# Kernel tuning notes

Measured on AMD Instinct MI355X. Metric: run time of the kernel, lower is better.

The kernel has to match this reference:

```python
import jax, jax.numpy as jnp
import numpy as np

HID = 32          # PositionalEncodingFourier hidden_dim
PE_TEMP = 10000.0


def _layer_norm(x, w, b):
    m = jnp.mean(x, -1, keepdims=True)
    v = jnp.mean((x - m) ** 2, -1, keepdims=True)
    return (x - m) / jnp.sqrt(v + 1e-6) * w + b


def _dwconv(x, w, b):
    # x: (B,C,H,W), w: (C,1,3,3) depthwise
    y = jax.lax.conv_general_dilated(x, w, (1, 1), 'SAME',
                                     feature_group_count=x.shape[1],
                                     dimension_numbers=('NCHW', 'OIHW', 'NCHW'))
    return y + b[None, :, None, None]


def _pos_embed(B, H, W, pw, pb):
    scale = 2 * np.pi
    eps = 1e-6
    dim_t = PE_TEMP ** (2 * (jnp.arange(HID) // 2).astype(jnp.float32) / HID)

    def four(e):  # e: (M,) -> (M,HID), interleaved sin/cos
        p = e[:, None] / dim_t
        return jnp.stack([jnp.sin(p[:, 0::2]), jnp.cos(p[:, 1::2])], -1).reshape(e.shape[0], HID)

    ye = jnp.arange(1, H + 1, dtype=jnp.float32) / (H + eps) * scale
    xe = jnp.arange(1, W + 1, dtype=jnp.float32) / (W + eps) * scale
    py = jnp.broadcast_to(four(ye)[:, None, :], (H, W, HID))
    px = jnp.broadcast_to(four(xe)[None, :, :], (H, W, HID))
    pos = jnp.concatenate([py, px], -1) @ pw.T + pb     # (H,W,C)
    C = pos.shape[-1]
    return jnp.broadcast_to(pos[None], (B, H, W, C)).reshape(B, H * W, C)


def _l2norm(x):
    return x / jnp.maximum(jnp.linalg.norm(x, axis=-1, keepdims=True), 1e-12)


def setup_inputs() -> dict:
    key = jax.random.key(0)
    ks = jax.random.split(key, 10)
    B, C, H, W = 32, 384, 32, 32
    nh, hid = 6, 6 * C
    f32 = jnp.float32
    d = {
        'x': jax.random.normal(ks[0], (B, C, H, W), f32),
        'pos_w': 0.02 * jax.random.normal(ks[1], (C, 2 * HID), f32),
        'pos_b': jnp.zeros((C,), f32),
        'ln1_w': jnp.ones((C,), f32), 'ln1_b': jnp.zeros((C,), f32),
        'q_w': 0.02 * jax.random.normal(ks[2], (C, C), f32), 'q_b': jnp.zeros((C,), f32),
        'k_w': 0.02 * jax.random.normal(ks[3], (C, C), f32), 'k_b': jnp.zeros((C,), f32),
        'vc_w': 0.02 * jax.random.normal(ks[4], (C, C), f32), 'vc_b': jnp.zeros((C,), f32),
        'dw_w': 0.1 * jax.random.normal(ks[5], (C, 1, 3, 3), f32), 'dw_b': jnp.zeros((C,), f32),
        'bn_g': jnp.ones((C,), f32), 'bn_b': jnp.zeros((C,), f32),
        'bn_mean': jnp.zeros((C,), f32), 'bn_var': jnp.ones((C,), f32),
        'temp': jnp.ones((nh, 1, 1), f32),
        'proj_w': 0.02 * jax.random.normal(ks[6], (C, C), f32), 'proj_b': jnp.zeros((C,), f32),
        'gamma1': jnp.full((C,), 1e-6, f32),
        'ln2_w': jnp.ones((C,), f32), 'ln2_b': jnp.zeros((C,), f32),
        'mlp_w1': 0.02 * jax.random.normal(ks[7], (hid, C), f32), 'mlp_b1': jnp.zeros((hid,), f32),
        'mlp_dw': 0.1 * jax.random.normal(ks[8], (hid, 1, 3, 3), f32), 'mlp_db': jnp.zeros((hid,), f32),
        'mlp_w2': 0.02 * jax.random.normal(ks[9], (C, hid), f32), 'mlp_b2': jnp.zeros((C,), f32),
        'gamma2': jnp.full((C,), 1e-6, f32),
    }
    return d


def reference(x, pos_w, pos_b, ln1_w, ln1_b, q_w, q_b, k_w, k_b, vc_w, vc_b,
              dw_w, dw_b, bn_g, bn_b, bn_mean, bn_var, temp, proj_w, proj_b,
              gamma1, ln2_w, ln2_b, mlp_w1, mlp_b1, mlp_dw, mlp_db,
              mlp_w2, mlp_b2, gamma2):
    B, C, H, W = x.shape
    N = H * W
    nh = temp.shape[0]
    dh = C // nh

    xf = x.reshape(B, C, N).transpose(0, 2, 1)          # (B,N,C)
    xf = xf + _pos_embed(B, H, W, pos_w, pos_b)
    xn = _layer_norm(xf, ln1_w, ln1_b)                  # (B,N,C)
    xs = xn.transpose(0, 2, 1).reshape(B, C, H, W)      # spatial view for DWConv

    # --- GLGXCA: channel-wise cross-covariance attention ---
    q = (xn @ q_w.T + q_b).reshape(B, N, nh, dh).transpose(0, 2, 3, 1)  # (B,h,d,N)
    k = (xn @ k_w.T + k_b).reshape(B, N, nh, dh).transpose(0, 2, 3, 1)
    q = _l2norm(q)
    k = _l2norm(k)
    attn = jnp.einsum('bhdn,bhen->bhde', q, k) * temp   # (B,h,d,d)
    attn = jax.nn.softmax(attn, axis=-1)

    vg = _dwconv(xs, dw_w, dw_b)
    vg = (vg - bn_mean[None, :, None, None]) / jnp.sqrt(bn_var + 1e-5)[None, :, None, None] \
         * bn_g[None, :, None, None] + bn_b[None, :, None, None]
    vg = vg * jax.nn.sigmoid(vg)                        # SiLU
    vg = vg.transpose(0, 2, 3, 1).reshape(B, N, C)
    vc = xn @ vc_w.T + vc_b
    v = (vc * vg).reshape(B, N, nh, dh).transpose(0, 2, 3, 1)           # (B,h,d,N)

    xo = jnp.einsum('bhde,bhen->bhdn', attn, v)         # (B,h,d,N)
    xo = xo.transpose(0, 3, 1, 2).reshape(B, N, C)
    xo = xo @ proj_w.T + proj_b
    xo = xo.reshape(B, H, W, C).transpose(0, 3, 1, 2)   # (B,C,H,W)

    # --- residual 1 (faithful: torch does transpose(1,2).reshape on BCHW) ---
    xa = xo * gamma1[None, :, None, None]
    xa = jnp.swapaxes(xa, 1, 2).reshape(B, C, H, W)
    x = x + xa

    # --- MLP branch ---
    xn2 = _layer_norm(x.transpose(0, 2, 3, 1), ln2_w, ln2_b).transpose(0, 3, 1, 2)
    h1 = jnp.einsum('bchw,oc->bohw', xn2, mlp_w1) + mlp_b1[None, :, None, None]
    h1 = jax.nn.gelu(h1, approximate=False)
    h2 = jax.nn.gelu(_dwconv(h1, mlp_dw, mlp_db), approximate=False)
    h3 = jnp.einsum('bchw,oc->bohw', h2, mlp_w2) + mlp_b2[None, :, None, None]
    return x + h3 * gamma2[None, :, None, None]
```

## Files before the change

### kernel.cpp

```cpp
#include <hip/hip_runtime.h>
#include <cstdint>
#include <cstddef>
#include <cmath>

#define DI __device__ __forceinline__

typedef __attribute__((ext_vector_type(2))) float f32x2;
typedef __attribute__((ext_vector_type(4))) float f32x4;
typedef __attribute__((ext_vector_type(8))) __bf16 bf16x8;
typedef __attribute__((ext_vector_type(4))) unsigned short u16x4;

constexpr int B_ = 32, C_ = 384, N_ = 1024, HID2_ = 2304, QS_ = 1152;

DI unsigned short f2b(float f) {
  union { float f; unsigned int u; } v; v.f = f;
  unsigned int u = v.u;
  return (unsigned short)((u + 0x7FFFu + ((u >> 16) & 1u)) >> 16);
}
DI float b2f(unsigned short h) {
  union { unsigned int u; float f; } v; v.u = ((unsigned int)h) << 16;
  return v.f;
}
DI float sigmoid_f(float x) { return __builtin_amdgcn_rcpf(1.0f + __expf(-x)); }
DI float gelu_f(float x) { return x * sigmoid_f(1.702f * x); }

DI void gload_lds16(const void* g, void* l) {
  __builtin_amdgcn_global_load_lds(
      (const __attribute__((address_space(1))) void*)g,
      (__attribute__((address_space(3))) void*)l, 16, 0, 0);
}

#if __has_builtin(__builtin_amdgcn_cvt_pk_fp8_f32) && __has_builtin(__builtin_amdgcn_cvt_pk_f32_fp8)
#define HW_FP8 1
#else
#define HW_FP8 0
#endif

DI unsigned char f2e4_sw(float x) {
  float a = fabsf(x);
  unsigned char s = (x < 0.f) ? 0x80 : 0;
  if (!(a >= 0.0009765625f)) return s;
  if (a >= 448.f) return s | 0x7E;
  int e; float m = frexpf(a, &e);
  m *= 2.f; e -= 1;
  if (e < -6) {
    int q = (int)rintf(a * 512.f);
    if (q > 7) return s | 0x08;
    return s | (unsigned char)q;
  }
  int mi = (int)rintf((m - 1.f) * 8.f);
  if (mi == 8) { mi = 0; e += 1; }
  if (e > 8) return s | 0x7E;
  return s | (unsigned char)(((e + 7) << 3) | mi);
}
DI float e42f_sw(unsigned char h) {
  int e = (h >> 3) & 0xF, m = h & 7;
  float v;
  if (e == 0) v = (float)m * 0.001953125f;
  else { union { unsigned u; float f; } w; w.u = (unsigned)((e + 120) << 23) | ((unsigned)m << 20); v = w.f; }
  return (h & 0x80) ? -v : v;
}
DI unsigned char f2e4(float x) {
#if HW_FP8
  int r = __builtin_amdgcn_cvt_pk_fp8_f32(x, x, 0, false);
  return (unsigned char)(r & 0xFF);
#else
  return f2e4_sw(x);
#endif
}
DI unsigned int enc4(float a, float b, float c, float d) {
#if HW_FP8
  int r = 0;
  r = __builtin_amdgcn_cvt_pk_fp8_f32(a, b, r, false);
  r = __builtin_amdgcn_cvt_pk_fp8_f32(c, d, r, true);
  return (unsigned int)r;
#else
  return (unsigned)f2e4(a) | ((unsigned)f2e4(b) << 8) | ((unsigned)f2e4(c) << 16) | ((unsigned)f2e4(d) << 24);
#endif
}
DI void dec4(unsigned int v, float* o) {
#if HW_FP8
  f32x2 lo = __builtin_amdgcn_cvt_pk_f32_fp8((int)v, false);
  f32x2 hi = __builtin_amdgcn_cvt_pk_f32_fp8((int)v, true);
  o[0] = lo[0]; o[1] = lo[1]; o[2] = hi[0]; o[3] = hi[1];
#else
  o[0] = e42f_sw(v & 0xFF); o[1] = e42f_sw((v >> 8) & 0xFF);
  o[2] = e42f_sw((v >> 16) & 0xFF); o[3] = e42f_sw((v >> 24) & 0xFF);
#endif
}

__global__ void prep_k(const float* __restrict__ q_w, const float* __restrict__ k_w,
    const float* __restrict__ vc_w, const float* __restrict__ pj_w,
    const float* __restrict__ w1, const float* __restrict__ w2,
    const float* __restrict__ dw_w, const float* __restrict__ mdw,
    const float* __restrict__ q_b, const float* __restrict__ k_b, const float* __restrict__ v_b,
    unsigned char* __restrict__ WQKV, unsigned char* __restrict__ WP,
    unsigned char* __restrict__ W1, unsigned char* __restrict__ W2,
    float* __restrict__ DT1, float* __restrict__ DT2,
    float* __restrict__ BQKV, float* __restrict__ feat) {
  int i = blockIdx.x * 256 + threadIdx.x;
  if (i < 442368) {
    int o = i / 384, c = i % 384;
    float v = (o < 384) ? q_w[o * 384 + c] : (o < 768) ? k_w[(o - 384) * 384 + c]
                                                       : vc_w[(o - 768) * 384 + c];
    WQKV[i] = f2e4(v); return;
  }
  i -= 442368;
  if (i < 147456) { WP[i] = f2e4(pj_w[i]); return; }
  i -= 147456;
  if (i < 884736) { W1[i] = f2e4(w1[i]); return; }
  i -= 884736;
  if (i < 884736) { W2[i] = f2e4(w2[i]); return; }
  i -= 884736;
  if (i < 3456)  { int c = i / 9, k = i % 9; DT1[k * C_ + c] = dw_w[i]; return; }
  i -= 3456;
  if (i < 20736) { int c = i / 9, k = i % 9; DT2[k * HID2_ + c] = mdw[i]; return; }
  i -= 20736;
  if (i < 1152)  { BQKV[i] = (i < 384) ? q_b[i] : (i < 768) ? k_b[i - 384] : v_b[i - 768]; return; }
  i -= 1152;
  if (i < 65536) {
    int n = i >> 6, j = i & 63;
    int h = n >> 5, w = n & 31;
    const float scale = 6.283185307179586f;
    float e = (j < 32) ? (float)(h + 1) / (32.0f + 1e-6f) * scale
                       : (float)(w + 1) / (32.0f + 1e-6f) * scale;
    int jj = j & 31;
    float dt = powf(10000.0f, (float)(jj >> 1) * (1.0f / 16.0f));
    float arg = e / dt;
    feat[i] = (jj & 1) ? cosf(arg) : sinf(arg);
  }
}

__global__ __launch_bounds__(384) void pos_k(const float* __restrict__ feat,
    const float* __restrict__ pw, const float* __restrict__ pb, float* __restrict__ pos) {
  __shared__ float fs[64];
  int n = blockIdx.x, c = threadIdx.x;
  if (c < 64) fs[c] = feat[n * 64 + c];
  __syncthreads();
  float s = pb[c];
  #pragma unroll
  for (int j = 0; j < 64; ++j) s += fs[j] * pw[c * 64 + j];
  pos[(size_t)n * C_ + c] = s;
}

template<int HASPOS>
__global__ __launch_bounds__(256) void ln_k(const float* __restrict__ xin,
    const float* __restrict__ pos, const float* __restrict__ lw,
    const float* __restrict__ lb, unsigned char* __restrict__ out8) {
  __shared__ float tile[C_ * 33];
  int bid = blockIdx.x;
  int b = bid >> 5, n0 = (bid & 31) << 5;
  int t = threadIdx.x;
  const float* xb = xin + (size_t)b * C_ * N_;
  #pragma unroll
  for (int i = 0; i < 48; ++i) {
    int f = t + 256 * i;
    int c = f >> 5, nn = f & 31;
    tile[c * 33 + nn] = xb[(size_t)c * N_ + n0 + nn];
  }
  __syncthreads();
  int wv = t >> 6, l = t & 63;
  for (int tk = 0; tk < 8; ++tk) {
    int tn = wv * 8 + tk;
    float v[6];
    #pragma unroll
    for (int i = 0; i < 6; ++i) {
      int c = l + 64 * i;
      float x = tile[c * 33 + tn];
      if (HASPOS) x += pos[(size_t)(n0 + tn) * C_ + c];
      v[i] = x;
    }
    float s = v[0] + v[1] + v[2] + v[3] + v[4] + v[5];
    #pragma unroll
    for (int m = 1; m < 64; m <<= 1) s += __shfl_xor(s, m);
    float mean = s * (1.0f / 384.0f);
    float q = 0.f;
    #pragma unroll
    for (int i = 0; i < 6; ++i) { float d = v[i] - mean; q += d * d; }
    #pragma unroll
    for (int m = 1; m < 64; m <<= 1) q += __shfl_xor(q, m);
    float rstd = rsqrtf(q * (1.0f / 384.0f) + 1e-6f);
    #pragma unroll
    for (int i = 0; i < 6; ++i) {
      int c = l + 64 * i;
      out8[((size_t)b * N_ + n0 + tn) * C_ + c] = f2e4((v[i] - mean) * rstd * lw[c] + lb[c]);
    }
  }
}

template<int EPI>
__global__ __launch_bounds__(256) void gemm8_k(const unsigned char* __restrict__ A,
    const unsigned char* __restrict__ Wt, const float* __restrict__ bias,
    unsigned char* __restrict__ out8, unsigned short* __restrict__ outb,
    int K, int O) {
  __shared__ __align__(16) unsigned char As[2][128 * 128];
  __shared__ __align__(16) unsigned char Bs[2][128 * 128];
  const int gx = gridDim.x;
  const int nwg = gx * gridDim.y;
  const int lid = blockIdx.y * gx + blockIdx.x;
  const int chunk = nwg >> 3;
  const int swz = (lid & 7) * chunk + (lid >> 3);
  const int m0 = (swz / gx) * 128, n0 = (swz % gx) * 128;
  const int t = threadIdx.x, l = t & 63, wv = t >> 6;
  const int wr = wv >> 1, wc = wv & 1;
  const int fr = l & 15, fq = l >> 4;
  const int arow = t >> 3;
  const int acsw = ((t & 7) ^ (arow & 7)) * 16;
  const unsigned char* Ag = A + (size_t)(m0 + arow) * K + acsw;
  const unsigned char* Bg = Wt + (size_t)(n0 + arow) * K + acsw;
  f32x4 acc[4][4];
  #pragma unroll
  for (int i = 0; i < 4; ++i)
    #pragma unroll
    for (int j = 0; j < 4; ++j) acc[i][j] = f32x4{0.f, 0.f, 0.f, 0.f};

  auto stage = [&](int buf, int k0) {
    char* Ad = (char*)&As[buf][0] + wv * 1024;
    char* Bd = (char*)&Bs[buf][0] + wv * 1024;
    #pragma unroll
    for (int s = 0; s < 4; ++s) {
      gload_lds16(Ag + (size_t)(s * 32) * K + k0, Ad + s * 4096);
      gload_lds16(Bg + (size_t)(s * 32) * K + k0, Bd + s * 4096);
    }
  };

  const int nt = K >> 7;
  stage(0, 0);
  for (int tt = 0; tt < nt; ++tt) {
    const int cur = tt & 1;
    if (tt + 1 < nt) {
      stage(cur ^ 1, (tt + 1) << 7);
      asm volatile("s_waitcnt vmcnt(8)" ::: "memory");
    } else {
      asm volatile("s_waitcnt vmcnt(0)" ::: "memory");
    }
    __builtin_amdgcn_s_barrier();
    #pragma unroll
    for (int kk = 0; kk < 4; ++kk) {
      const int slot = (kk << 1) | (fq >> 1);
      const int sub = (fq & 1) << 3;
      long af[4], bfr[4];
      #pragma unroll
      for (int mi = 0; mi < 4; ++mi) {
        int row = wr * 64 + mi * 16 + fr;
        af[mi] = *(const long*)((const char*)&As[cur][0] + row * 128 +
                                ((slot ^ (row & 7)) << 4) + sub);
      }
      #pragma unroll
      for (int ni = 0; ni < 4; ++ni) {
        int row = wc * 64 + ni * 16 + fr;
        bfr[ni] = *(const long*)((const char*)&Bs[cur][0] + row * 128 +
                                 ((slot ^ (row & 7)) << 4) + sub);
      }
      #pragma unroll
      for (int mi = 0; mi < 4; ++mi)
        #pragma unroll
        for (int ni = 0; ni < 4; ++ni)
          acc[mi][ni] = __builtin_amdgcn_mfma_f32_16x16x32_fp8_fp8(af[mi], bfr[ni], acc[mi][ni], 0, 0, 0);
    }
    __builtin_amdgcn_s_barrier();
  }
  const int rb = fq * 4;
  #pragma unroll
  for (int mi = 0; mi < 4; ++mi) {
    #pragma unroll
    for (int ni = 0; ni < 4; ++ni) {
      int col = n0 + wc * 64 + ni * 16 + fr;
      float bv = bias[col];
      #pragma unroll
      for (int j = 0; j < 4; ++j) {
        int row = m0 + wr * 64 + mi * 16 + rb + j;
        float val = acc[mi][ni][j] + bv;
        if (EPI == 0)      out8[(size_t)row * O + col] = f2e4(val);
        else if (EPI == 1) out8[(size_t)row * O + col] = f2e4(gelu_f(val));
        else               outb[(size_t)row * O + col] = f2b(val);
      }
    }
  }
}

__global__ __launch_bounds__(256) void fc2t8_k(const unsigned char* __restrict__ W2b,
    const unsigned char* __restrict__ H2, const float* __restrict__ b2,
    const float* __restrict__ g2, float* __restrict__ out, int bofs) {
  __shared__ __align__(16) unsigned char As[2][128 * 128];
  __shared__ __align__(16) unsigned char Bs[2][128 * 128];
  const int K = HID2_;
  const int nwg = 8 * gridDim.y;
  const int lid = blockIdx.y * 8 + blockIdx.x;
  const int chunk = nwg >> 3;
  const int swz = (lid & 7) * chunk + (lid >> 3);
  const int n0 = (swz & 7) * 128;
  const int y2 = swz >> 3;
  const int img = y2 / 3, m0 = (y2 % 3) * 128;
  const int t = threadIdx.x, l = t & 63, wv = t >> 6;
  const int wr = wv >> 1, wc = wv & 1;
  const int fr = l & 15, fq = l >> 4;
  const int arow = t >> 3;
  const int acsw = ((t & 7) ^ (arow & 7)) * 16;
  const unsigned char* Ag = W2b + (size_t)(m0 + arow) * K + acsw;
  const unsigned char* Bg = H2 + ((size_t)img * N_ + n0 + arow) * K + acsw;
  f32x4 acc[4][4];
  #pragma unroll
  for (int i = 0; i < 4; ++i)
    #pragma unroll
    for (int j = 0; j < 4; ++j) acc[i][j] = f32x4{0.f, 0.f, 0.f, 0.f};

  auto stage = [&](int buf, int k0) {
    char* Ad = (char*)&As[buf][0] + wv * 1024;
    char* Bd = (char*)&Bs[buf][0] + wv * 1024;
    #pragma unroll
    for (int s = 0; s < 4; ++s) {
      gload_lds16(Ag + (size_t)(s * 32) * K + k0, Ad + s * 4096);
      gload_lds16(Bg + (size_t)(s * 32) * K + k0, Bd + s * 4096);
    }
  };

  const int nt = K >> 7;
  stage(0, 0);
  for (int tt = 0; tt < nt; ++tt) {
    const int cur = tt & 1;
    if (tt + 1 < nt) {
      stage(cur ^ 1, (tt + 1) << 7);
      asm volatile("s_waitcnt vmcnt(8)" ::: "memory");
    } else {
      asm volatile("s_waitcnt vmcnt(0)" ::: "memory");
    }
    __builtin_amdgcn_s_barrier();
    #pragma unroll
    for (int kk = 0; kk < 4; ++kk) {
      const int slot = (kk << 1) | (fq >> 1);
      const int sub = (fq & 1) << 3;
      long af[4], bfr[4];
      #pragma unroll
      for (int mi = 0; mi < 4; ++mi) {
        int row = wr * 64 + mi * 16 + fr;
        af[mi] = *(const long*)((const char*)&As[cur][0] + row * 128 +
                                ((slot ^ (row & 7)) << 4) + sub);
      }
      #pragma unroll
      for (int ni = 0; ni < 4; ++ni) {
        int row = wc * 64 + ni * 16 + fr;
        bfr[ni] = *(const long*)((const char*)&Bs[cur][0] + row * 128 +
                                 ((slot ^ (row & 7)) << 4) + sub);
      }
      #pragma unroll
      for (int mi = 0; mi < 4; ++mi)
        #pragma unroll
        for (int ni = 0; ni < 4; ++ni)
          acc[mi][ni] = __builtin_amdgcn_mfma_f32_16x16x32_fp8_fp8(af[mi], bfr[ni], acc[mi][ni], 0, 0, 0);
    }
    __builtin_amdgcn_s_barrier();
  }
  const int rb = fq * 4;
  const size_t obase = ((size_t)(img + bofs) * C_) << 10;
  #pragma unroll
  for (int mi = 0; mi < 4; ++mi) {
    #pragma unroll
    for (int j = 0; j < 4; ++j) {
      int row = m0 + wr * 64 + mi * 16 + rb + j;
      float bv = b2[row], gv = g2[row];
      #pragma unroll
      for (int ni = 0; ni < 4; ++ni) {
        int col = n0 + wc * 64 + ni * 16 + fr;
        size_t oi = obase + ((size_t)row << 10) + col;
        out[oi] = out[oi] + gv * (acc[mi][ni][j] + bv);
      }
    }
  }
}

__global__ __launch_bounds__(256) void attn_k(const unsigned char* __restrict__ qkv,
    const float* __restrict__ temp, unsigned char* __restrict__ attn8) {
  __shared__ __align__(16) float Qs[32][68];
  __shared__ __align__(16) float Ks[32][68];
  __shared__ float qinv_s[64], kinv_s[64];
  const int bid = blockIdx.x;
  const int b = bid / 6, h = bid % 6;
  const int t = threadIdx.x;
  const unsigned char* qb = qkv + (size_t)b * N_ * QS_ + h * 64;
  const unsigned char* kb = qb + 384;
  const int li = t >> 4, ld = (t & 15) * 4;
  const int d0 = (t >> 4) * 4, e0 = (t & 15) * 4;
  float acc[4][4] = {};
  float ssq = 0.0f;
  for (int n0 = 0; n0 < N_; n0 += 32) {
    __syncthreads();
    #pragma unroll
    for (int rr = 0; rr < 2; ++rr) {
      int i = li + rr * 16;
      unsigned int qv = *(const unsigned int*)(qb + (size_t)(n0 + i) * QS_ + ld);
      unsigned int kv = *(const unsigned int*)(kb + (size_t)(n0 + i) * QS_ + ld);
      float qd[4], kd[4];
      dec4(qv, qd); dec4(kv, kd);
      #pragma unroll
      for (int j = 0; j < 4; ++j) { Qs[i][ld + j] = qd[j]; Ks[i][ld + j] = kd[j]; }
    }
    __syncthreads();
    if (t < 64) {
      #pragma unroll
      for (int i = 0; i < 32; ++i) { float x = Qs[i][t]; ssq += x * x; }
    } else if (t < 128) {
      #pragma unroll
      for (int i = 0; i < 32; ++i) { float x = Ks[i][t - 64]; ssq += x * x; }
    }
    #pragma unroll
    for (int i = 0; i < 32; ++i) {
      f32x4 qv = *(const f32x4*)&Qs[i][d0];
      f32x4 kv = *(const f32x4*)&Ks[i][e0];
      #pragma unroll
      for (int di = 0; di < 4; ++di)
        #pragma unroll
        for (int ei = 0; ei < 4; ++ei) acc[di][ei] += qv[di] * kv[ei];
    }
  }
  if (t < 64) { float nr = sqrtf(ssq); qinv_s[t] = 1.0f / fmaxf(nr, 1e-12f); }
  else if (t < 128) { float nr = sqrtf(ssq); kinv_s[t - 64] = 1.0f / fmaxf(nr, 1e-12f); }
  __syncthreads();
  const float tp = temp[h];
  #pragma unroll
  for (int di = 0; di < 4; ++di) {
    int d = d0 + di;
    float vals[4];
    #pragma unroll
    for (int ei = 0; ei < 4; ++ei) vals[ei] = acc[di][ei] * qinv_s[d] * kinv_s[e0 + ei] * tp;
    float mx = fmaxf(fmaxf(vals[0], vals[1]), fmaxf(vals[2], vals[3]));
    #pragma unroll
    for (int m = 1; m < 16; m <<= 1) mx = fmaxf(mx, __shfl_xor(mx, m));
    float ex[4], s = 0.f;
    #pragma unroll
    for (int ei = 0; ei < 4; ++ei) { ex[ei] = __expf(vals[ei] - mx); s += ex[ei]; }
    #pragma unroll
    for (int m = 1; m < 16; m <<= 1) s += __shfl_xor(s, m);
    float inv = __builtin_amdgcn_rcpf(s);
    unsigned int ov = enc4(ex[0] * inv, ex[1] * inv, ex[2] * inv, ex[3] * inv);
    *(unsigned int*)(attn8 + ((size_t)(b * 6 + h) * 64 + d) * 64 + e0) = ov;
  }
}

__global__ __launch_bounds__(192) void dwconv1_k(const unsigned char* __restrict__ xn,
    const float* __restrict__ dwt, const float* __restrict__ dwb,
    const float* __restrict__ bng, const float* __restrict__ bnb,
    const float* __restrict__ bnm, const float* __restrict__ bnv,
    unsigned char* __restrict__ qkv) {
  const int c0 = threadIdx.x * 4;
  const int h = blockIdx.y >> 2;
  const int w0 = (blockIdx.y & 3) * 8 + threadIdx.y * 4;
  const int b = blockIdx.z;
  const unsigned char* xb = xn + ((size_t)b * N_ + h * 32) * C_ + c0;
  f32x4 acc[4] = {};
  #pragma unroll
  for (int dy = -1; dy <= 1; ++dy) {
    int hh = h + dy;
    if (hh < 0 || hh >= 32) continue;
    f32x4 xf[6];
    #pragma unroll
    for (int j = 0; j < 6; ++j) {
      int ww = w0 - 1 + j;
      if (ww >= 0 && ww < 32) {
        unsigned int xv = *(const unsigned int*)(xb + (dy * 32 + ww) * C_);
        float d4[4]; dec4(xv, d4);
        xf[j] = f32x4{d4[0], d4[1], d4[2], d4[3]};
      } else xf[j] = f32x4{0.f, 0.f, 0.f, 0.f};
    }
    #pragma unroll
    for (int dx = 0; dx < 3; ++dx) {
      f32x4 wv = *(const f32x4*)(dwt + ((dy + 1) * 3 + dx) * C_ + c0);
      #pragma unroll
      for (int px = 0; px < 4; ++px)
        #pragma unroll
        for (int j = 0; j < 4; ++j) acc[px][j] += xf[dx + px][j] * wv[j];
    }
  }
  f32x4 dbv = *(const f32x4*)(dwb + c0);
  f32x4 mv = *(const f32x4*)(bnm + c0);
  f32x4 vv = *(const f32x4*)(bnv + c0);
  f32x4 gv = *(const f32x4*)(bng + c0);
  f32x4 bv = *(const f32x4*)(bnb + c0);
  f32x4 rs;
  #pragma unroll
  for (int j = 0; j < 4; ++j) rs[j] = rsqrtf(vv[j] + 1e-5f);
  unsigned char* vb = qkv + ((size_t)b * N_ + h * 32 + w0) * QS_ + 768 + c0;
  #pragma unroll
  for (int px = 0; px < 4; ++px) {
    unsigned int vcv = *(const unsigned int*)(vb + px * QS_);
    float vd[4]; dec4(vcv, vd);
    float o4[4];
    #pragma unroll
    for (int j = 0; j < 4; ++j) {
      float u = (acc[px][j] + dbv[j] - mv[j]) * rs[j] * gv[j] + bv[j];
      float si = u * sigmoid_f(u);
      o4[j] = si * vd[j];
    }
    *(unsigned int*)(vb + px * QS_) = enc4(o4[0], o4[1], o4[2], o4[3]);
  }
}

__global__ __launch_bounds__(256) void xo_k(const unsigned char* __restrict__ qkv,
    const unsigned char* __restrict__ attn, unsigned char* __restrict__ xo) {
  const int bid = blockIdx.x;
  const int b = bid / 96, r = bid % 96, h = r / 16, m0 = (r % 16) * 64;
  const int t = threadIdx.x, wv = t >> 6, l = t & 63;
  const int n0 = m0 + wv * 16;
  const int fr = l & 15, fq = l >> 4;
  const unsigned char* vb = qkv + (size_t)b * N_ * QS_ + 768 + h * 64;
  const unsigned char* ab = attn + (size_t)(b * 6 + h) * 4096;
  f32x4 acc[4];
  #pragma unroll
  for (int i = 0; i < 4; ++i) acc[i] = f32x4{0.f, 0.f, 0.f, 0.f};
  #pragma unroll
  for (int k0 = 0; k0 < 64; k0 += 32) {
    long af = *(const long*)(vb + (size_t)(n0 + fr) * QS_ + k0 + fq * 8);
    #pragma unroll
    for (int ni = 0; ni < 4; ++ni) {
      long bfr = *(const long*)(ab + (ni * 16 + fr) * 64 + k0 + fq * 8);
      acc[ni] = __builtin_amdgcn_mfma_f32_16x16x32_fp8_fp8(af, bfr, acc[ni], 0, 0, 0);
    }
  }
  const int rb = fq * 4;
  #pragma unroll
  for (int ni = 0; ni < 4; ++ni)
    #pragma unroll
    for (int j = 0; j < 4; ++j) {
      int row = n0 + rb + j;
      xo[((size_t)b * N_ + row) * C_ + h * 64 + ni * 16 + fr] = f2e4(acc[ni][j]);
    }
}

__global__ __launch_bounds__(256) void resid1_k(const float* __restrict__ x,
    const unsigned short* __restrict__ y, const float* __restrict__ g1,
    float* __restrict__ xnew) {
  __shared__ unsigned short yp[32][36];
  __shared__ float g1s[32];
  const int bid = blockIdx.x;
  const int b = bid / C_, c2 = bid % C_;
  const int hsrc = c2 / 12, cs0 = (c2 % 12) * 32;
  const int t = threadIdx.x;
  {
    int wq = t >> 3, h4 = (t & 7) * 4;
    u16x4 vv = *(const u16x4*)(y + ((size_t)b * N_ + hsrc * 32 + wq) * C_ + cs0 + h4);
    *(u16x4*)&yp[wq][h4] = vv;
  }
  if (t < 32) g1s[t] = g1[cs0 + t];
  __syncthreads();
  int h2 = t >> 3, w0 = (t & 7) * 4;
  size_t base = (((size_t)b * C_ + c2) << 10) + h2 * 32 + w0;
  f32x4 xv = *(const f32x4*)(x + base);
  f32x4 ov;
  #pragma unroll
  for (int i = 0; i < 4; ++i) ov[i] = xv[i] + g1s[h2] * b2f(yp[w0 + i][h2]);
  *(f32x4*)(xnew + base) = ov;
}

__global__ __launch_bounds__(192) void dwconv2_k(const unsigned char* __restrict__ h1,
    const float* __restrict__ dwt, const float* __restrict__ dwb,
    unsigned char* __restrict__ h2) {
  const int c0 = (blockIdx.x * 192 + threadIdx.x) * 4;
  const int h = blockIdx.y >> 3, w0 = (blockIdx.y & 7) * 4;
  const int b = blockIdx.z;
  const unsigned char* xb = h1 + ((size_t)b * N_ + h * 32) * HID2_ + c0;
  f32x4 acc[4] = {};
  #pragma unroll
  for (int dy = -1; dy <= 1; ++dy) {
    int hh = h + dy;
    if (hh < 0 || hh >= 32) continue;
    f32x4 xf[6];
    #pragma unroll
    for (int j = 0; j < 6; ++j) {
      int ww = w0 - 1 + j;
      if (ww >= 0 && ww < 32) {
        unsigned int xv = *(const unsigned int*)(xb + (dy * 32 + ww) * HID2_);
        float d4[4]; dec4(xv, d4);
        xf[j] = f32x4{d4[0], d4[1], d4[2], d4[3]};
      } else xf[j] = f32x4{0.f, 0.f, 0.f, 0.f};
    }
    #pragma unroll
    for (int dx = 0; dx < 3; ++dx) {
      f32x4 wv = *(const f32x4*)(dwt + ((dy + 1) * 3 + dx) * HID2_ + c0);
      #pragma unroll
      for (int px = 0; px < 4; ++px)
        #pragma unroll
        for (int j = 0; j < 4; ++j) acc[px][j] += xf[dx + px][j] * wv[j];
    }
  }
  f32x4 dbv = *(const f32x4*)(dwb + c0);
  unsigned char* ob = h2 + ((size_t)b * N_ + h * 32 + w0) * HID2_ + c0;
  #pragma unroll
  for (int px = 0; px < 4; ++px) {
    unsigned int ov = enc4(gelu_f(acc[px][0] + dbv[0]), gelu_f(acc[px][1] + dbv[1]),
                           gelu_f(acc[px][2] + dbv[2]), gelu_f(acc[px][3] + dbv[3]));
    *(unsigned int*)(ob + px * HID2_) = ov;
  }
}

extern "C" void kernel_launch(void* const* d_in, const int* in_sizes, int n_in,
                              void* d_out, int out_size, void* d_ws, size_t ws_size,
                              hipStream_t stream) {
  (void)in_sizes; (void)n_in; (void)out_size;
  const float* x    = (const float*)d_in[0];
  const float* posw = (const float*)d_in[1];
  const float* posb = (const float*)d_in[2];
  const float* ln1w = (const float*)d_in[3];
  const float* ln1b = (const float*)d_in[4];
  const float* q_w  = (const float*)d_in[5];
  const float* q_b  = (const float*)d_in[6];
  const float* k_w  = (const float*)d_in[7];
  const float* k_b  = (const float*)d_in[8];
  const float* v_w  = (const float*)d_in[9];
  const float* v_b  = (const float*)d_in[10];
  const float* dw_w = (const float*)d_in[11];
  const float* dw_b = (const float*)d_in[12];
  const float* bn_g = (const float*)d_in[13];
  const float* bn_b = (const float*)d_in[14];
  const float* bn_m = (const float*)d_in[15];
  const float* bn_v = (const float*)d_in[16];
  const float* temp = (const float*)d_in[17];
  const float* pj_w = (const float*)d_in[18];
  const float* pj_b = (const float*)d_in[19];
  const float* g1   = (const float*)d_in[20];
  const float* ln2w = (const float*)d_in[21];
  const float* ln2b = (const float*)d_in[22];
  const float* w1   = (const float*)d_in[23];
  const float* b1   = (const float*)d_in[24];
  const float* mdw  = (const float*)d_in[25];
  const float* mdb  = (const float*)d_in[26];
  const float* w2   = (const float*)d_in[27];
  const float* b2   = (const float*)d_in[28];
  const float* g2   = (const float*)d_in[29];
  float* out = (float*)d_out;

  char* ws = (char*)d_ws;
  size_t off = 0;
  auto alloc = [&](size_t bytes) { size_t o = off; off += (bytes + 255) & ~(size_t)255; return o; };
  const size_t TOK = (size_t)B_ * N_;

  size_t oWQKV = alloc(442368), oWP = alloc(147456);
  size_t oW1 = alloc(884736), oW2 = alloc(884736);
  size_t oDT1 = alloc(9 * C_ * 4), oDT2 = alloc(9 * HID2_ * 4);
  size_t oBQKV = alloc(1152 * 4);
  size_t oFEAT = alloc(65536 * 4);
  size_t oPOS  = alloc((size_t)N_ * C_ * 4);
  size_t oATT  = alloc((size_t)B_ * 6 * 4096);
  size_t oXN2  = alloc(TOK * C_);
  size_t oQKV  = alloc(TOK * QS_);
  size_t oXN = alloc(TOK * C_);
  size_t oSC = alloc(TOK * C_);
  size_t oSA = alloc(TOK * C_ * 2);

  const size_t perImg = (size_t)N_ * HID2_;
  size_t avail = (ws_size > oQKV + 512) ? (ws_size - oQKV - 512) : 0;
  int CH = (int)(avail / (2 * perImg));
  if (CH < 1) CH = 1;
  if (CH > 32) CH = 32;
  size_t oH1 = oQKV;
  size_t oH2 = oQKV + (size_t)CH * perImg;

  unsigned char* WQKV = (unsigned char*)(ws + oWQKV);
  unsigned char* WP = (unsigned char*)(ws + oWP);
  unsigned char* W1 = (unsigned char*)(ws + oW1);
  unsigned char* W2 = (unsigned char*)(ws + oW2);
  float* DT1 = (float*)(ws + oDT1);
  float* DT2 = (float*)(ws + oDT2);
  float* BQKV = (float*)(ws + oBQKV);
  float* FEAT = (float*)(ws + oFEAT);
  float* POS  = (float*)(ws + oPOS);
  unsigned char* ATT = (unsigned char*)(ws + oATT);
  unsigned char* XN2 = (unsigned char*)(ws + oXN2);
  unsigned char* QKV = (unsigned char*)(ws + oQKV);
  unsigned char* XN = (unsigned char*)(ws + oXN);
  unsigned char* SC = (unsigned char*)(ws + oSC);
  unsigned short* SA = (unsigned short*)(ws + oSA);
  unsigned char* H1 = (unsigned char*)(ws + oH1);
  unsigned char* H2 = (unsigned char*)(ws + oH2);

  prep_k<<<9571, 256, 0, stream>>>(q_w, k_w, v_w, pj_w, w1, w2, dw_w, mdw,
                                   q_b, k_b, v_b, WQKV, WP, W1, W2, DT1, DT2, BQKV, FEAT);
  pos_k<<<1024, 384, 0, stream>>>(FEAT, posw, posb, POS);
  ln_k<1><<<1024, 256, 0, stream>>>(x, POS, ln1w, ln1b, XN);
  gemm8_k<0><<<dim3(9, 256), 256, 0, stream>>>(XN, WQKV, BQKV, QKV, nullptr, 384, 1152);
  attn_k<<<192, 256, 0, stream>>>(QKV, temp, ATT);
  dwconv1_k<<<dim3(1, 128, 32), dim3(96, 2), 0, stream>>>(XN, DT1, dw_b, bn_g, bn_b, bn_m, bn_v, QKV);
  xo_k<<<3072, 256, 0, stream>>>(QKV, ATT, SC);
  gemm8_k<2><<<dim3(3, 256), 256, 0, stream>>>(SC, WP, pj_b, nullptr, SA, 384, 384);
  resid1_k<<<12288, 256, 0, stream>>>(x, SA, g1, out);
  ln_k<0><<<1024, 256, 0, stream>>>(out, nullptr, ln2w, ln2b, XN2);
  for (int b0 = 0; b0 < B_; b0 += CH) {
    int cb = (b0 + CH <= B_) ? CH : (B_ - b0);
    const unsigned char* xn2c = XN2 + (size_t)b0 * N_ * C_;
    gemm8_k<1><<<dim3(18, cb * 8), 256, 0, stream>>>(xn2c, W1, b1, H1, nullptr, 384, 2304);
    dwconv2_k<<<dim3(3, 256, cb), 192, 0, stream>>>(H1, DT2, mdb, H2);
    fc2t8_k<<<dim3(8, 3 * cb), 256, 0, stream>>>(W2, H2, b2, g2, out, b0);
  }
}
```

Baseline: 452.6 us.

## Halve FP8 GEMM K-tile and stage fp8 epilogue through LDS for coalesced stores

The FP8 GEMM K-step drops from 128 to 64 bytes, which halves LDS per workgroup (32KB total) so more workgroups can be resident. The swizzle and wait counts are adjusted to match. For the fp8-output epilogues, the byte-scattered global stores are replaced by writing the tile into LDS and then copying it out with 16-byte vector stores. The cost is twice as many loop iterations and barriers, plus one extra barrier and an LDS round trip in the epilogue.

Measured after the change: 474.6 us. +4.9%, slower.

```diff
diff --git a/kernel.cpp b/kernel.cpp
--- a/kernel.cpp
+++ b/kernel.cpp
@@ -7,7 +7,7 @@
 
 typedef __attribute__((ext_vector_type(2))) float f32x2;
 typedef __attribute__((ext_vector_type(4))) float f32x4;
-typedef __attribute__((ext_vector_type(8))) __bf16 bf16x8;
+typedef __attribute__((ext_vector_type(4))) unsigned int u32x4;
 typedef __attribute__((ext_vector_type(4))) unsigned short u16x4;
 
 constexpr int B_ = 32, C_ = 384, N_ = 1024, HID2_ = 2304, QS_ = 1152;
@@ -193,8 +193,8 @@
     const unsigned char* __restrict__ Wt, const float* __restrict__ bias,
     unsigned char* __restrict__ out8, unsigned short* __restrict__ outb,
     int K, int O) {
-  __shared__ __align__(16) unsigned char As[2][128 * 128];
-  __shared__ __align__(16) unsigned char Bs[2][128 * 128];
+  __shared__ __align__(16) unsigned char As[2][128 * 64];
+  __shared__ __align__(16) unsigned char Bs[2][128 * 64];
   const int gx = gridDim.x;
   const int nwg = gx * gridDim.y;
   const int lid = blockIdx.y * gx + blockIdx.x;
@@ -204,8 +204,8 @@
   const int t = threadIdx.x, l = t & 63, wv = t >> 6;
   const int wr = wv >> 1, wc = wv & 1;
   const int fr = l & 15, fq = l >> 4;
-  const int arow = t >> 3;
-  const int acsw = ((t & 7) ^ (arow & 7)) * 16;
+  const int arow = t >> 2;
+  const int acsw = ((t & 3) ^ (arow & 3)) * 16;
   const unsigned char* Ag = A + (size_t)(m0 + arow) * K + acsw;
   const unsigned char* Bg = Wt + (size_t)(n0 + arow) * K + acsw;
   f32x4 acc[4][4];
@@ -217,40 +217,39 @@
   auto stage = [&](int buf, int k0) {
     char* Ad = (char*)&As[buf][0] + wv * 1024;
     char* Bd = (char*)&Bs[buf][0] + wv * 1024;
-    #pragma unroll
-    for (int s = 0; s < 4; ++s) {
-      gload_lds16(Ag + (size_t)(s * 32) * K + k0, Ad + s * 4096);
-      gload_lds16(Bg + (size_t)(s * 32) * K + k0, Bd + s * 4096);
-    }
+    gload_lds16(Ag + k0, Ad);
+    gload_lds16(Ag + (size_t)64 * K + k0, Ad + 4096);
+    gload_lds16(Bg + k0, Bd);
+    gload_lds16(Bg + (size_t)64 * K + k0, Bd + 4096);
   };
 
-  const int nt = K >> 7;
+  const int nt = K >> 6;
   stage(0, 0);
   for (int tt = 0; tt < nt; ++tt) {
     const int cur = tt & 1;
     if (tt + 1 < nt) {
-      stage(cur ^ 1, (tt + 1) << 7);
-      asm volatile("s_waitcnt vmcnt(8)" ::: "memory");
+      stage(cur ^ 1, (tt + 1) << 6);
+      asm volatile("s_waitcnt vmcnt(4)" ::: "memory");
     } else {
       asm volatile("s_waitcnt vmcnt(0)" ::: "memory");
     }
     __builtin_amdgcn_s_barrier();
     #pragma unroll
-    for (int kk = 0; kk < 4; ++kk) {
+    for (int kk = 0; kk < 2; ++kk) {
       const int slot = (kk << 1) | (fq >> 1);
       const int sub = (fq & 1) << 3;
       long af[4], bfr[4];
       #pragma unroll
       for (int mi = 0; mi < 4; ++mi) {
         int row = wr * 64 + mi * 16 + fr;
-        af[mi] = *(const long*)((const char*)&As[cur][0] + row * 128 +
-                                ((slot ^ (row & 7)) << 4) + sub);
+        af[mi] = *(const long*)((const char*)&As[cur][0] + row * 64 +
+                                ((slot ^ (row & 3)) << 4) + sub);
       }
       #pragma unroll
       for (int ni = 0; ni < 4; ++ni) {
         int row = wc * 64 + ni * 16 + fr;
-        bfr[ni] = *(const long*)((const char*)&Bs[cur][0] + row * 128 +
-                                 ((slot ^ (row & 7)) << 4) + sub);
+        bfr[ni] = *(const long*)((const char*)&Bs[cur][0] + row * 64 +
+                                 ((slot ^ (row & 3)) << 4) + sub);
       }
       #pragma unroll
       for (int mi = 0; mi < 4; ++mi)
@@ -261,21 +260,43 @@
     __builtin_amdgcn_s_barrier();
   }
   const int rb = fq * 4;
-  #pragma unroll
-  for (int mi = 0; mi < 4; ++mi) {
-    #pragma unroll
-    for (int ni = 0; ni < 4; ++ni) {
-      int col = n0 + wc * 64 + ni * 16 + fr;
-      float bv = bias[col];
-      #pragma unroll
-      for (int j = 0; j < 4; ++j) {
-        int row = m0 + wr * 64 + mi * 16 + rb + j;
-        float val = acc[mi][ni][j] + bv;
-        if (EPI == 0)      out8[(size_t)row * O + col] = f2e4(val);
-        else if (EPI == 1) out8[(size_t)row * O + col] = f2e4(gelu_f(val));
-        else               outb[(size_t)row * O + col] = f2b(val);
+  if (EPI == 2) {
+    #pragma unroll
+    for (int mi = 0; mi < 4; ++mi)
+      #pragma unroll
+      for (int ni = 0; ni < 4; ++ni) {
+        int col = n0 + wc * 64 + ni * 16 + fr;
+        float bv = bias[col];
+        #pragma unroll
+        for (int j = 0; j < 4; ++j) {
+          int row = m0 + wr * 64 + mi * 16 + rb + j;
+          outb[(size_t)row * O + col] = f2b(acc[mi][ni][j] + bv);
+        }
       }
-    }
+  } else {
+    unsigned char* ctile = (unsigned char*)&As[0][0];
+    #pragma unroll
+    for (int mi = 0; mi < 4; ++mi) {
+      #pragma unroll
+      for (int ni = 0; ni < 4; ++ni) {
+        int lcol = wc * 64 + ni * 16 + fr;
+        float bv = bias[n0 + lcol];
+        #pragma unroll
+        for (int j = 0; j < 4; ++j) {
+          int lrow = wr * 64 + mi * 16 + rb + j;
+          float val = acc[mi][ni][j] + bv;
+          if (EPI == 1) val = gelu_f(val);
+          ctile[lrow * 128 + lcol] = f2e4(val);
+        }
+      }
+    }
+    __builtin_amdgcn_s_barrier();
+    const int row = t >> 1, off = (t & 1) * 64;
+    const char* src = (const char*)ctile + row * 128 + off;
+    unsigned char* dst = out8 + (size_t)(m0 + row) * O + n0 + off;
+    #pragma unroll
+    for (int q = 0; q < 4; ++q)
+      *(u32x4*)(dst + q * 16) = *(const u32x4*)(src + q * 16);
   }
 }
 
```
